# Optimization experiments

Hardware: AMD Instinct MI355X
Metric: run time of the kernel (lower is better)

## Reference

```python
import jax, jax.numpy as jnp
import numpy as np

NUM_NODES = 100000
NUM_EDGES = 1600000
INPUT_DIM = 128
HIDDEN_DIM = 64
OUTPUT_DIM = 2
DROPOUT_P = 0.5


def setup_inputs() -> dict:
    key = jax.random.key(0)
    ks = jax.random.split(key, 6)
    x = jax.random.normal(ks[0], (NUM_NODES, INPUT_DIM), dtype=jnp.float32)
    edge_index = jax.random.randint(ks[1], (2, NUM_EDGES), 0, NUM_NODES, dtype=jnp.int64)
    W_conv = jax.random.normal(ks[2], (INPUT_DIM, HIDDEN_DIM), dtype=jnp.float32) * (1.0 / np.sqrt(INPUT_DIM))
    b_conv = jax.random.normal(ks[3], (HIDDEN_DIM,), dtype=jnp.float32) * 0.02
    W_lin = jax.random.normal(ks[4], (HIDDEN_DIM, OUTPUT_DIM), dtype=jnp.float32) * (1.0 / np.sqrt(HIDDEN_DIM))
    b_lin = jax.random.normal(ks[5], (OUTPUT_DIM,), dtype=jnp.float32) * 0.02
    return {"x": x, "edge_index": edge_index, "W_conv": W_conv, "b_conv": b_conv,
            "W_lin": W_lin, "b_lin": b_lin}


def _gcn_conv(x, edge_index, W, b):
    n = x.shape[0]
    # linear transform first (PyG GCNConv)
    h = x @ W  # [N, hidden]
    # add self-loops
    loop = jnp.arange(n, dtype=edge_index.dtype)
    row = jnp.concatenate([edge_index[0], loop])  # source
    col = jnp.concatenate([edge_index[1], loop])  # target
    # symmetric normalization deg^{-1/2} (degree counted on targets, incl. self-loops)
    deg = jax.ops.segment_sum(jnp.ones_like(col, dtype=h.dtype), col, num_segments=n)
    dinv = jnp.where(deg > 0, jax.lax.rsqrt(deg), 0.0)
    norm = dinv[row] * dinv[col]  # [E+N]
    # gather -> scale -> scatter-add
    msgs = h[row] * norm[:, None]  # [E+N, hidden]
    out = jax.ops.segment_sum(msgs, col, num_segments=n)
    return out + b


def reference(x, edge_index, W_conv, b_conv, W_lin, b_lin):
    h = _gcn_conv(x, edge_index, W_conv, b_conv)
    h = jax.nn.relu(h)
    # dropout p=0.5, training mode, deterministic key for reproducibility
    keep = jax.random.bernoulli(jax.random.key(42), 1.0 - DROPOUT_P, h.shape)
    h = jnp.where(keep, h / (1.0 - DROPOUT_P), 0.0)
    return h @ W_lin + b_lin
```

## Files before the change

### kernel.cpp

```cpp
#include <hip/hip_runtime.h>
#include <hip/hip_bf16.h>

#define N_NODES 100000
#define N_EDGES 1600000
#define IN_DIM 128
#define HID 64
#define NB ((N_NODES + 255) / 256)
#define EPB 4096
#define BUCKET_BLOCKS ((N_EDGES + EPB - 1) / EPB)
#define MAXPB 8192

typedef __attribute__((ext_vector_type(8))) short bf16x8;
typedef __attribute__((ext_vector_type(4))) float f32x4;

__device__ __forceinline__ unsigned rotl32(unsigned x, unsigned r) {
    return (x << r) | (x >> (32u - r));
}

__device__ __forceinline__ void threefry2x32_k42(unsigned x0, unsigned x1,
                                                 unsigned& o0, unsigned& o1) {
    const unsigned ks0 = 0u;
    const unsigned ks1 = 42u;
    const unsigned ks2 = 0u ^ 42u ^ 0x1BD11BDAu;
    x0 += ks0; x1 += ks1;
    x0 += x1; x1 = rotl32(x1, 13); x1 ^= x0;
    x0 += x1; x1 = rotl32(x1, 15); x1 ^= x0;
    x0 += x1; x1 = rotl32(x1, 26); x1 ^= x0;
    x0 += x1; x1 = rotl32(x1, 6);  x1 ^= x0;
    x0 += ks1; x1 += ks2 + 1u;
    x0 += x1; x1 = rotl32(x1, 17); x1 ^= x0;
    x0 += x1; x1 = rotl32(x1, 29); x1 ^= x0;
    x0 += x1; x1 = rotl32(x1, 16); x1 ^= x0;
    x0 += x1; x1 = rotl32(x1, 24); x1 ^= x0;
    x0 += ks2; x1 += ks0 + 2u;
    x0 += x1; x1 = rotl32(x1, 13); x1 ^= x0;
    x0 += x1; x1 = rotl32(x1, 15); x1 ^= x0;
    x0 += x1; x1 = rotl32(x1, 26); x1 ^= x0;
    x0 += x1; x1 = rotl32(x1, 6);  x1 ^= x0;
    x0 += ks0; x1 += ks1 + 3u;
    x0 += x1; x1 = rotl32(x1, 17); x1 ^= x0;
    x0 += x1; x1 = rotl32(x1, 29); x1 ^= x0;
    x0 += x1; x1 = rotl32(x1, 16); x1 ^= x0;
    x0 += x1; x1 = rotl32(x1, 24); x1 ^= x0;
    x0 += ks1; x1 += ks2 + 4u;
    x0 += x1; x1 = rotl32(x1, 13); x1 ^= x0;
    x0 += x1; x1 = rotl32(x1, 15); x1 ^= x0;
    x0 += x1; x1 = rotl32(x1, 26); x1 ^= x0;
    x0 += x1; x1 = rotl32(x1, 6);  x1 ^= x0;
    x0 += ks2; x1 += ks0 + 5u;
    o0 = x0; o1 = x1;
}

__device__ __forceinline__ float bf2f(unsigned short u) {
    return __uint_as_float((unsigned)u << 16);
}
__device__ __forceinline__ float bf2f_lo(unsigned u) {
    return __uint_as_float(u << 16);
}
__device__ __forceinline__ float bf2f_hi(unsigned u) {
    return __uint_as_float(u & 0xffff0000u);
}

__global__ __launch_bounds__(512) void k_bucket(const int* __restrict__ src,
                                                const int* __restrict__ dst,
                                                int* __restrict__ bucketcnt,
                                                unsigned* __restrict__ gbuf) {
    __shared__ int cnt[512];
    __shared__ int off[512];
    __shared__ int cur[NB];
    __shared__ int gbase[NB];
    __shared__ unsigned buf[EPB];
    __shared__ unsigned short bkt[EPB];
    const int t = threadIdx.x;
    const int e0 = blockIdx.x * EPB;
    const int n = min(EPB, N_EDGES - e0);
    cnt[t] = 0;
    __syncthreads();
    unsigned myrec[EPB / 512];
    int myb[EPB / 512];
#pragma unroll
    for (int k = 0; k < EPB / 512; k++) {
        int e = e0 + k * 512 + t;
        if (e < N_EDGES) {
            int r = src[e];
            int c = dst[e];
            int b = c >> 8;
            myrec[k] = ((unsigned)(c & 255) << 17) | (unsigned)r;
            myb[k] = b;
            atomicAdd(&cnt[b], 1);
        } else {
            myb[k] = -1;
        }
    }
    __syncthreads();
    int own = cnt[t];
    for (int o = 1; o < 512; o <<= 1) {
        int v = (t >= o) ? cnt[t - o] : 0;
        __syncthreads();
        cnt[t] += v;
        __syncthreads();
    }
    off[t] = cnt[t] - own;
    if (t < NB) {
        cur[t] = off[t];
        gbase[t] = t * MAXPB + (own ? atomicAdd(&bucketcnt[t], own) : 0);
    }
    __syncthreads();
#pragma unroll
    for (int k = 0; k < EPB / 512; k++) {
        if (myb[k] >= 0) {
            int p = atomicAdd(&cur[myb[k]], 1);
            buf[p] = myrec[k];
            bkt[p] = (unsigned short)myb[k];
        }
    }
    __syncthreads();
    for (int j = t; j < n; j += 512) {
        int b = bkt[j];
        gbuf[gbase[b] + (j - off[b])] = buf[j];
    }
}

__global__ __launch_bounds__(512) void k_scanB(const int* __restrict__ bucketcnt,
                                               int* __restrict__ bucket_base) {
    __shared__ int s[512];
    int t = threadIdx.x;
    int own = (t < NB) ? bucketcnt[t] : 0;
    s[t] = own;
    __syncthreads();
    for (int o = 1; o < 512; o <<= 1) {
        int v = (t >= o) ? s[t - o] : 0;
        __syncthreads();
        s[t] += v;
        __syncthreads();
    }
    if (t < NB) bucket_base[t] = s[t] - own;
    if (t == 511) bucket_base[NB] = s[511];
}

__global__ __launch_bounds__(256) void k_csr2(const unsigned* __restrict__ gbuf,
                                              const int* __restrict__ bucketcnt,
                                              const int* __restrict__ bucket_base,
                                              int* __restrict__ row_start,
                                              float* __restrict__ dinv,
                                              int* __restrict__ srcs) {
    __shared__ unsigned lbuf[MAXPB];
    __shared__ int lcnt[256];
    __shared__ int pre[256];
    __shared__ int cur[256];
    const int b = blockIdx.x, t = threadIdx.x;
    const int n = bucketcnt[b];
    const unsigned* reg = gbuf + (size_t)b * MAXPB;
    lcnt[t] = 0;
    for (int j = t; j < n; j += 256) lbuf[j] = reg[j];
    __syncthreads();
    for (int j = t; j < n; j += 256) atomicAdd(&lcnt[lbuf[j] >> 17], 1);
    __syncthreads();
    int my = lcnt[t];
    pre[t] = my;
    __syncthreads();
    for (int o = 1; o < 256; o <<= 1) {
        int v = (t >= o) ? pre[t - o] : 0;
        __syncthreads();
        pre[t] += v;
        __syncthreads();
    }
    const int gb = bucket_base[b];
    int base = gb + pre[t] - my;
    cur[t] = base;
    const int c = b * 256 + t;
    if (c < N_NODES) {
        row_start[c] = base;
        dinv[c] = rsqrtf((float)(my + 1));
    }
    if (b == NB - 1 && t == 255) row_start[N_NODES] = gb + pre[255];
    __syncthreads();
    for (int j = t; j < n; j += 256) {
        unsigned rec = lbuf[j];
        int pos = atomicAdd(&cur[rec >> 17], 1);
        srcs[pos] = (int)(rec & 0x1FFFF);
    }
}

__global__ __launch_bounds__(256) void k_gemm(const float* __restrict__ x,
                                              const float* __restrict__ W,
                                              const float* __restrict__ dinv,
                                              unsigned short* __restrict__ gm) {
    __shared__ unsigned short WtH[HID][136];
    __shared__ unsigned short WtL[HID][136];
    const int t = threadIdx.x;
    {
        const int n = t & 63;
        const int k0 = (t >> 6) * 32;
        for (int k = k0; k < k0 + 32; k += 2) {
            float w0 = W[(size_t)k * HID + n];
            float w1 = W[(size_t)(k + 1) * HID + n];
            unsigned short h0 = __bfloat16_as_ushort(__float2bfloat16(w0));
            unsigned short h1 = __bfloat16_as_ushort(__float2bfloat16(w1));
            unsigned short l0 = __bfloat16_as_ushort(__float2bfloat16(w0 - bf2f(h0)));
            unsigned short l1 = __bfloat16_as_ushort(__float2bfloat16(w1 - bf2f(h1)));
            *(unsigned*)&WtH[n][k] = (unsigned)h0 | ((unsigned)h1 << 16);
            *(unsigned*)&WtL[n][k] = (unsigned)l0 | ((unsigned)l1 << 16);
        }
    }
    __syncthreads();

    const int wave = t >> 6, lane = t & 63;
    const int row16 = lane & 15;
    const int kgrp = lane >> 4;
    const int browA = blockIdx.x * 64 + wave * 16;

    const int rA = min(browA + row16, N_NODES - 1);
    const float* xr = x + (size_t)rA * IN_DIM + kgrp * 8;
    float xv[32];
#pragma unroll
    for (int ks = 0; ks < 4; ks++) {
        *(f32x4*)&xv[ks * 8]     = *(const f32x4*)(xr + ks * 32);
        *(f32x4*)&xv[ks * 8 + 4] = *(const f32x4*)(xr + ks * 32 + 4);
    }
    bf16x8 ah[4], al[4];
#pragma unroll
    for (int ks = 0; ks < 4; ks++) {
#pragma unroll
        for (int j = 0; j < 8; j++) {
            float v = xv[ks * 8 + j];
            unsigned short h = __bfloat16_as_ushort(__float2bfloat16(v));
            unsigned short l = __bfloat16_as_ushort(__float2bfloat16(v - bf2f(h)));
            ah[ks][j] = (short)h;
            al[ks][j] = (short)l;
        }
    }

    float dv[4];
    int orow[4];
#pragma unroll
    for (int i = 0; i < 4; i++) {
        orow[i] = browA + kgrp * 4 + i;
        dv[i] = dinv[min(orow[i], N_NODES - 1)];
    }

#pragma unroll
    for (int nt = 0; nt < 4; nt++) {
        const int n = nt * 16 + row16;
        bf16x8 bh[4], bl[4];
#pragma unroll
        for (int ks = 0; ks < 4; ks++) {
            bh[ks] = *(const bf16x8*)&WtH[n][ks * 32 + kgrp * 8];
            bl[ks] = *(const bf16x8*)&WtL[n][ks * 32 + kgrp * 8];
        }
        f32x4 acc = {0.f, 0.f, 0.f, 0.f};
#pragma unroll
        for (int ks = 0; ks < 4; ks++)
            acc = __builtin_amdgcn_mfma_f32_16x16x32_bf16(ah[ks], bh[ks], acc, 0, 0, 0);
#pragma unroll
        for (int ks = 0; ks < 4; ks++)
            acc = __builtin_amdgcn_mfma_f32_16x16x32_bf16(al[ks], bh[ks], acc, 0, 0, 0);
#pragma unroll
        for (int ks = 0; ks < 4; ks++)
            acc = __builtin_amdgcn_mfma_f32_16x16x32_bf16(ah[ks], bl[ks], acc, 0, 0, 0);
#pragma unroll
        for (int i = 0; i < 4; i++) {
            if (orow[i] < N_NODES) {
                float g = acc[i] * dv[i];
                gm[(size_t)orow[i] * HID + nt * 16 + row16] =
                    __bfloat16_as_ushort(__float2bfloat16(g));
            }
        }
    }
}

__global__ __launch_bounds__(256, 4) void k_aggr(const unsigned short* __restrict__ gm,
                                                 const int* __restrict__ row_start,
                                                 const int* __restrict__ srcs,
                                                 const float* __restrict__ dinv,
                                                 const float* __restrict__ bconv,
                                                 const float* __restrict__ Wlin,
                                                 const float* __restrict__ blin,
                                                 float* __restrict__ out) {
    const int c  = blockIdx.x * 16 + (threadIdx.x >> 4);
    const int d4 = threadIdx.x & 15;
    const int beg = row_start[c];
    const int end = row_start[c + 1];

    const uint2 s0 = *(const uint2*)(gm + ((size_t)c << 6) + (d4 << 2));
    float a0 = bf2f_lo(s0.x), a1 = bf2f_hi(s0.x);
    float a2 = bf2f_lo(s0.y), a3 = bf2f_hi(s0.y);

#define LOADG(ri) (*(const uint2*)(gm + ((size_t)(ri) << 6) + (d4 << 2)))

    if (beg < end) {
        const int last = end - 1;
        int r[8];
        uint2 wa[8], wb[8];
#pragma unroll
        for (int u = 0; u < 8; u++) r[u] = srcs[min(beg + u, last)];
#pragma unroll
        for (int u = 0; u < 8; u++) wa[u] = LOADG(r[u]);
        bool haveB = (beg + 8 < end);
        if (haveB) {
#pragma unroll
            for (int u = 0; u < 8; u++) r[u] = srcs[min(beg + 8 + u, last)];
#pragma unroll
            for (int u = 0; u < 8; u++) wb[u] = LOADG(r[u]);
        }
        int j = beg;
        while (true) {
#pragma unroll
            for (int u = 0; u < 8; u++) {
                const unsigned m = (j + u < end) ? 0xffffffffu : 0u;
                a0 += bf2f_lo(wa[u].x & m); a1 += bf2f_hi(wa[u].x & m);
                a2 += bf2f_lo(wa[u].y & m); a3 += bf2f_hi(wa[u].y & m);
            }
            j += 8;
            if (!haveB) break;
            const bool haveN = (j + 8 < end);
            if (haveN) {
#pragma unroll
                for (int u = 0; u < 8; u++) r[u] = srcs[min(j + 8 + u, last)];
#pragma unroll
                for (int u = 0; u < 8; u++) wa[u] = LOADG(r[u]);
            }
#pragma unroll
            for (int u = 0; u < 8; u++) {
                const unsigned m = (j + u < end) ? 0xffffffffu : 0u;
                a0 += bf2f_lo(wb[u].x & m); a1 += bf2f_hi(wb[u].x & m);
                a2 += bf2f_lo(wb[u].y & m); a3 += bf2f_hi(wb[u].y & m);
            }
            j += 8;
            if (!haveN) break;
            haveB = (j + 8 < end);
            if (haveB) {
#pragma unroll
                for (int u = 0; u < 8; u++) r[u] = srcs[min(j + 8 + u, last)];
#pragma unroll
                for (int u = 0; u < 8; u++) wb[u] = LOADG(r[u]);
            }
        }
    }
#undef LOADG

    const float dv = dinv[c];
    const float4 bc4 = *(const float4*)(bconv + (d4 << 2));
    float v0 = fmaxf(a0 * dv + bc4.x, 0.f);
    float v1 = fmaxf(a1 * dv + bc4.y, 0.f);
    float v2 = fmaxf(a2 * dv + bc4.z, 0.f);
    float v3 = fmaxf(a3 * dv + bc4.w, 0.f);

    const unsigned ib = (unsigned)(c * HID + (d4 << 2));
    unsigned o0, o1;
    threefry2x32_k42(0u, ib + 0u, o0, o1);
    v0 = ((o0 ^ o1) & 0x80000000u) ? 0.f : v0 * 2.f;
    threefry2x32_k42(0u, ib + 1u, o0, o1);
    v1 = ((o0 ^ o1) & 0x80000000u) ? 0.f : v1 * 2.f;
    threefry2x32_k42(0u, ib + 2u, o0, o1);
    v2 = ((o0 ^ o1) & 0x80000000u) ? 0.f : v2 * 2.f;
    threefry2x32_k42(0u, ib + 3u, o0, o1);
    v3 = ((o0 ^ o1) & 0x80000000u) ? 0.f : v3 * 2.f;

    const float4 wl0 = *(const float4*)(Wlin + (d4 << 3));
    const float4 wl1 = *(const float4*)(Wlin + (d4 << 3) + 4);
    float p0 = v0 * wl0.x + v1 * wl0.z + v2 * wl1.x + v3 * wl1.z;
    float p1 = v0 * wl0.y + v1 * wl0.w + v2 * wl1.y + v3 * wl1.w;

#pragma unroll
    for (int off = 8; off; off >>= 1) {
        p0 += __shfl_xor(p0, off);
        p1 += __shfl_xor(p1, off);
    }
    if (d4 == 0) {
        *(float2*)(out + (size_t)c * 2) = make_float2(p0 + blin[0], p1 + blin[1]);
    }
}

extern "C" void kernel_launch(void* const* d_in, const int* in_sizes, int n_in,
                              void* d_out, int out_size, void* d_ws, size_t ws_size,
                              hipStream_t stream) {
    const float* x  = (const float*)d_in[0];
    const void*  ei = d_in[1];
    const float* Wc = (const float*)d_in[2];
    const float* bc = (const float*)d_in[3];
    const float* Wl = (const float*)d_in[4];
    const float* bl = (const float*)d_in[5];
    for (int i = 0; i < n_in; i++) {
        switch (in_sizes[i]) {
            case N_NODES * IN_DIM:   x  = (const float*)d_in[i]; break;
            case 2 * N_EDGES:
            case 4 * N_EDGES:        ei = d_in[i]; break;
            case IN_DIM * HID:       Wc = (const float*)d_in[i]; break;
            case HID:                bc = (const float*)d_in[i]; break;
            case HID * 2:            Wl = (const float*)d_in[i]; break;
            case 2:                  bl = (const float*)d_in[i]; break;
            default: break;
        }
    }
    float* out = (float*)d_out;

    const int* src = (const int*)ei;
    const int* dst = (const int*)ei + N_EDGES;

    char* ws = (char*)d_ws;
    size_t off = 0;
    unsigned short* gm    = (unsigned short*)(ws + off); off += (size_t)N_NODES * HID * 2;
    float*    dinv        = (float*)(ws + off);    off += (size_t)N_NODES * 4;
    int*      row_start   = (int*)(ws + off);      off += (size_t)(N_NODES + 4) * 4;
    int*      bucketcnt   = (int*)(ws + off);      off += (size_t)(NB + 4) * 4;
    int*      bucket_base = (int*)(ws + off);      off += (size_t)(NB + 4) * 4;
    unsigned* gbuf        = (unsigned*)(ws + off); off += (size_t)NB * MAXPB * 4;
    int*      srcs        = (int*)(ws + off);      off += (size_t)N_EDGES * 4;

    hipMemsetAsync(bucketcnt, 0, (size_t)NB * 4, stream);
    k_bucket<<<BUCKET_BLOCKS, 512, 0, stream>>>(src, dst, bucketcnt, gbuf);
    k_scanB<<<1, 512, 0, stream>>>(bucketcnt, bucket_base);
    k_csr2<<<NB, 256, 0, stream>>>(gbuf, bucketcnt, bucket_base, row_start, dinv, srcs);
    k_gemm<<<(N_NODES + 63) / 64, 256, 0, stream>>>(x, Wc, dinv, gm);
    k_aggr<<<(N_NODES + 15) / 16, 256, 0, stream>>>(gm, row_start, srcs, dinv, bc, Wl, bl, out);
}
```

Measured before the change: 184.2 us.

## Replace block-local bucket sort with global atomic sub-bucket scatter and in-place CSR

```diff
diff --git a/kernel.cpp b/kernel.cpp
--- a/kernel.cpp
+++ b/kernel.cpp
@@ -6,9 +6,9 @@
 #define IN_DIM 128
 #define HID 64
 #define NB ((N_NODES + 255) / 256)
-#define EPB 4096
-#define BUCKET_BLOCKS ((N_EDGES + EPB - 1) / EPB)
-#define MAXPB 8192
+#define NSUB 8
+#define SUBCAP 1024
+#define MAXPB (NSUB * SUBCAP)
 
 typedef __attribute__((ext_vector_type(8))) short bf16x8;
 typedef __attribute__((ext_vector_type(4))) float f32x4;
@@ -61,102 +61,54 @@
     return __uint_as_float(u & 0xffff0000u);
 }
 
-__global__ __launch_bounds__(512) void k_bucket(const int* __restrict__ src,
-                                                const int* __restrict__ dst,
-                                                int* __restrict__ bucketcnt,
-                                                unsigned* __restrict__ gbuf) {
-    __shared__ int cnt[512];
-    __shared__ int off[512];
-    __shared__ int cur[NB];
-    __shared__ int gbase[NB];
-    __shared__ unsigned buf[EPB];
-    __shared__ unsigned short bkt[EPB];
-    const int t = threadIdx.x;
-    const int e0 = blockIdx.x * EPB;
-    const int n = min(EPB, N_EDGES - e0);
-    cnt[t] = 0;
-    __syncthreads();
-    unsigned myrec[EPB / 512];
-    int myb[EPB / 512];
-#pragma unroll
-    for (int k = 0; k < EPB / 512; k++) {
-        int e = e0 + k * 512 + t;
-        if (e < N_EDGES) {
-            int r = src[e];
-            int c = dst[e];
-            int b = c >> 8;
-            myrec[k] = ((unsigned)(c & 255) << 17) | (unsigned)r;
-            myb[k] = b;
-            atomicAdd(&cnt[b], 1);
-        } else {
-            myb[k] = -1;
-        }
-    }
-    __syncthreads();
-    int own = cnt[t];
-    for (int o = 1; o < 512; o <<= 1) {
-        int v = (t >= o) ? cnt[t - o] : 0;
-        __syncthreads();
-        cnt[t] += v;
-        __syncthreads();
-    }
-    off[t] = cnt[t] - own;
-    if (t < NB) {
-        cur[t] = off[t];
-        gbase[t] = t * MAXPB + (own ? atomicAdd(&bucketcnt[t], own) : 0);
-    }
-    __syncthreads();
-#pragma unroll
-    for (int k = 0; k < EPB / 512; k++) {
-        if (myb[k] >= 0) {
-            int p = atomicAdd(&cur[myb[k]], 1);
-            buf[p] = myrec[k];
-            bkt[p] = (unsigned short)myb[k];
-        }
-    }
-    __syncthreads();
-    for (int j = t; j < n; j += 512) {
-        int b = bkt[j];
-        gbuf[gbase[b] + (j - off[b])] = buf[j];
-    }
-}
-
-__global__ __launch_bounds__(512) void k_scanB(const int* __restrict__ bucketcnt,
-                                               int* __restrict__ bucket_base) {
-    __shared__ int s[512];
-    int t = threadIdx.x;
-    int own = (t < NB) ? bucketcnt[t] : 0;
-    s[t] = own;
-    __syncthreads();
-    for (int o = 1; o < 512; o <<= 1) {
-        int v = (t >= o) ? s[t - o] : 0;
-        __syncthreads();
-        s[t] += v;
-        __syncthreads();
-    }
-    if (t < NB) bucket_base[t] = s[t] - own;
-    if (t == 511) bucket_base[NB] = s[511];
-}
-
-__global__ __launch_bounds__(256) void k_csr2(const unsigned* __restrict__ gbuf,
-                                              const int* __restrict__ bucketcnt,
-                                              const int* __restrict__ bucket_base,
-                                              int* __restrict__ row_start,
-                                              float* __restrict__ dinv,
-                                              int* __restrict__ srcs) {
+__global__ __launch_bounds__(256) void k_bucket2(const int* __restrict__ src,
+                                                 const int* __restrict__ dst,
+                                                 int* __restrict__ subcnt,
+                                                 unsigned* __restrict__ gbuf) {
+    const int gid = blockIdx.x * 256 + threadIdx.x;
+    const int e0 = gid * 4;
+    if (e0 >= N_EDGES) return;
+    const int4 s4 = *(const int4*)(src + e0);
+    const int4 d4 = *(const int4*)(dst + e0);
+    const int ss[4] = {s4.x, s4.y, s4.z, s4.w};
+    const int dd[4] = {d4.x, d4.y, d4.z, d4.w};
+#pragma unroll
+    for (int k = 0; k < 4; k++) {
+        const int b = dd[k] >> 8;
+        const int sub = (e0 + k) & (NSUB - 1);
+        const unsigned rec = ((unsigned)(dd[k] & 255) << 17) | (unsigned)ss[k];
+        const int p = atomicAdd(&subcnt[b * NSUB + sub], 1);
+        gbuf[(size_t)b * MAXPB + sub * SUBCAP + p] = rec;
+    }
+}
+
+__global__ __launch_bounds__(256) void k_csr3(unsigned* __restrict__ gbuf,
+                                              const int* __restrict__ subcnt,
+                                              int2* __restrict__ row_se,
+                                              float* __restrict__ dinv) {
     __shared__ unsigned lbuf[MAXPB];
     __shared__ int lcnt[256];
     __shared__ int pre[256];
     __shared__ int cur[256];
+    __shared__ int c8[NSUB + 1];
     const int b = blockIdx.x, t = threadIdx.x;
-    const int n = bucketcnt[b];
-    const unsigned* reg = gbuf + (size_t)b * MAXPB;
+    if (t == 0) {
+        int acc = 0;
+        for (int s = 0; s < NSUB; s++) { c8[s] = acc; acc += subcnt[b * NSUB + s]; }
+        c8[NSUB] = acc;
+    }
     lcnt[t] = 0;
-    for (int j = t; j < n; j += 256) lbuf[j] = reg[j];
+    __syncthreads();
+    for (int s = 0; s < NSUB; s++) {
+        const int n_s = c8[s + 1] - c8[s];
+        const unsigned* seg = gbuf + (size_t)b * MAXPB + s * SUBCAP;
+        for (int j = t; j < n_s; j += 256) lbuf[c8[s] + j] = seg[j];
+    }
+    const int n = c8[NSUB];
     __syncthreads();
     for (int j = t; j < n; j += 256) atomicAdd(&lcnt[lbuf[j] >> 17], 1);
     __syncthreads();
-    int my = lcnt[t];
+    const int my = lcnt[t];
     pre[t] = my;
     __syncthreads();
     for (int o = 1; o < 256; o <<= 1) {
@@ -165,20 +117,18 @@
         pre[t] += v;
         __syncthreads();
     }
-    const int gb = bucket_base[b];
-    int base = gb + pre[t] - my;
+    const int base = b * MAXPB + pre[t] - my;
     cur[t] = base;
     const int c = b * 256 + t;
     if (c < N_NODES) {
-        row_start[c] = base;
+        row_se[c] = make_int2(base, base + my);
         dinv[c] = rsqrtf((float)(my + 1));
     }
-    if (b == NB - 1 && t == 255) row_start[N_NODES] = gb + pre[255];
     __syncthreads();
     for (int j = t; j < n; j += 256) {
-        unsigned rec = lbuf[j];
-        int pos = atomicAdd(&cur[rec >> 17], 1);
-        srcs[pos] = (int)(rec & 0x1FFFF);
+        const unsigned rec = lbuf[j];
+        const int pos = atomicAdd(&cur[rec >> 17], 1);
+        ((int*)gbuf)[pos] = (int)(rec & 0x1FFFF);
     }
 }
 
@@ -270,7 +220,7 @@
 }
 
 __global__ __launch_bounds__(256, 4) void k_aggr(const unsigned short* __restrict__ gm,
-                                                 const int* __restrict__ row_start,
+                                                 const int2* __restrict__ row_se,
                                                  const int* __restrict__ srcs,
                                                  const float* __restrict__ dinv,
                                                  const float* __restrict__ bconv,
@@ -279,8 +229,9 @@
                                                  float* __restrict__ out) {
     const int c  = blockIdx.x * 16 + (threadIdx.x >> 4);
     const int d4 = threadIdx.x & 15;
-    const int beg = row_start[c];
-    const int end = row_start[c + 1];
+    const int2 se = row_se[c];
+    const int beg = se.x;
+    const int end = se.y;
 
     const uint2 s0 = *(const uint2*)(gm + ((size_t)c << 6) + (d4 << 2));
     float a0 = bf2f_lo(s0.x), a1 = bf2f_hi(s0.x);
@@ -400,18 +351,17 @@
 
     char* ws = (char*)d_ws;
     size_t off = 0;
-    unsigned short* gm    = (unsigned short*)(ws + off); off += (size_t)N_NODES * HID * 2;
-    float*    dinv        = (float*)(ws + off);    off += (size_t)N_NODES * 4;
-    int*      row_start   = (int*)(ws + off);      off += (size_t)(N_NODES + 4) * 4;
-    int*      bucketcnt   = (int*)(ws + off);      off += (size_t)(NB + 4) * 4;
-    int*      bucket_base = (int*)(ws + off);      off += (size_t)(NB + 4) * 4;
-    unsigned* gbuf        = (unsigned*)(ws + off); off += (size_t)NB * MAXPB * 4;
-    int*      srcs        = (int*)(ws + off);      off += (size_t)N_EDGES * 4;
-
-    hipMemsetAsync(bucketcnt, 0, (size_t)NB * 4, stream);
-    k_bucket<<<BUCKET_BLOCKS, 512, 0, stream>>>(src, dst, bucketcnt, gbuf);
-    k_scanB<<<1, 512, 0, stream>>>(bucketcnt, bucket_base);
-    k_csr2<<<NB, 256, 0, stream>>>(gbuf, bucketcnt, bucket_base, row_start, dinv, srcs);
+    unsigned short* gm = (unsigned short*)(ws + off); off += (size_t)N_NODES * HID * 2;
+    float* dinv        = (float*)(ws + off);   off += (size_t)N_NODES * 4;
+    int2*  row_se      = (int2*)(ws + off);    off += (size_t)N_NODES * 8;
+    int*   subcnt      = (int*)(ws + off);     off += (size_t)(NB * NSUB + 64) * 4;
+    off = (off + 255) & ~(size_t)255;
+    unsigned* gbuf     = (unsigned*)(ws + off); off += (size_t)NB * MAXPB * 4;
+
+    hipMemsetAsync(subcnt, 0, (size_t)NB * NSUB * 4, stream);
+    k_bucket2<<<(N_EDGES / 4 + 255) / 256, 256, 0, stream>>>(src, dst, subcnt, gbuf);
+    k_csr3<<<NB, 256, 0, stream>>>(gbuf, subcnt, row_se, dinv);
     k_gemm<<<(N_NODES + 63) / 64, 256, 0, stream>>>(x, Wc, dinv, gm);
-    k_aggr<<<(N_NODES + 15) / 16, 256, 0, stream>>>(gm, row_start, srcs, dinv, bc, Wl, bl, out);
-}
+    k_aggr<<<(N_NODES + 15) / 16, 256, 0, stream>>>(gm, row_se, (const int*)gbuf,
+                                                    dinv, bc, Wl, bl, out);
+}
```

New measurement: 310.3 us. 68.5% more time.

## Drop bucket scan kernel, build sparse CSR in place with start/end pairs

Applied to the files above, without the earlier changes.

```diff
diff --git a/kernel.cpp b/kernel.cpp
--- a/kernel.cpp
+++ b/kernel.cpp
@@ -121,29 +121,10 @@
     }
 }
 
-__global__ __launch_bounds__(512) void k_scanB(const int* __restrict__ bucketcnt,
-                                               int* __restrict__ bucket_base) {
-    __shared__ int s[512];
-    int t = threadIdx.x;
-    int own = (t < NB) ? bucketcnt[t] : 0;
-    s[t] = own;
-    __syncthreads();
-    for (int o = 1; o < 512; o <<= 1) {
-        int v = (t >= o) ? s[t - o] : 0;
-        __syncthreads();
-        s[t] += v;
-        __syncthreads();
-    }
-    if (t < NB) bucket_base[t] = s[t] - own;
-    if (t == 511) bucket_base[NB] = s[511];
-}
-
-__global__ __launch_bounds__(256) void k_csr2(const unsigned* __restrict__ gbuf,
+__global__ __launch_bounds__(256) void k_csr3(unsigned* __restrict__ gbuf,
                                               const int* __restrict__ bucketcnt,
-                                              const int* __restrict__ bucket_base,
-                                              int* __restrict__ row_start,
-                                              float* __restrict__ dinv,
-                                              int* __restrict__ srcs) {
+                                              int2* __restrict__ row_se,
+                                              float* __restrict__ dinv) {
     __shared__ unsigned lbuf[MAXPB];
     __shared__ int lcnt[256];
     __shared__ int pre[256];
@@ -156,7 +137,7 @@
     __syncthreads();
     for (int j = t; j < n; j += 256) atomicAdd(&lcnt[lbuf[j] >> 17], 1);
     __syncthreads();
-    int my = lcnt[t];
+    const int my = lcnt[t];
     pre[t] = my;
     __syncthreads();
     for (int o = 1; o < 256; o <<= 1) {
@@ -165,20 +146,18 @@
         pre[t] += v;
         __syncthreads();
     }
-    const int gb = bucket_base[b];
-    int base = gb + pre[t] - my;
+    const int base = b * MAXPB + pre[t] - my;
     cur[t] = base;
     const int c = b * 256 + t;
     if (c < N_NODES) {
-        row_start[c] = base;
+        row_se[c] = make_int2(base, base + my);
         dinv[c] = rsqrtf((float)(my + 1));
     }
-    if (b == NB - 1 && t == 255) row_start[N_NODES] = gb + pre[255];
     __syncthreads();
     for (int j = t; j < n; j += 256) {
-        unsigned rec = lbuf[j];
-        int pos = atomicAdd(&cur[rec >> 17], 1);
-        srcs[pos] = (int)(rec & 0x1FFFF);
+        const unsigned rec = lbuf[j];
+        const int pos = atomicAdd(&cur[rec >> 17], 1);
+        ((int*)gbuf)[pos] = (int)(rec & 0x1FFFF);
     }
 }
 
@@ -270,7 +249,7 @@
 }
 
 __global__ __launch_bounds__(256, 4) void k_aggr(const unsigned short* __restrict__ gm,
-                                                 const int* __restrict__ row_start,
+                                                 const int2* __restrict__ row_se,
                                                  const int* __restrict__ srcs,
                                                  const float* __restrict__ dinv,
                                                  const float* __restrict__ bconv,
@@ -279,8 +258,9 @@
                                                  float* __restrict__ out) {
     const int c  = blockIdx.x * 16 + (threadIdx.x >> 4);
     const int d4 = threadIdx.x & 15;
-    const int beg = row_start[c];
-    const int end = row_start[c + 1];
+    const int2 se = row_se[c];
+    const int beg = se.x;
+    const int end = se.y;
 
     const uint2 s0 = *(const uint2*)(gm + ((size_t)c << 6) + (d4 << 2));
     float a0 = bf2f_lo(s0.x), a1 = bf2f_hi(s0.x);
@@ -400,18 +380,17 @@
 
     char* ws = (char*)d_ws;
     size_t off = 0;
-    unsigned short* gm    = (unsigned short*)(ws + off); off += (size_t)N_NODES * HID * 2;
-    float*    dinv        = (float*)(ws + off);    off += (size_t)N_NODES * 4;
-    int*      row_start   = (int*)(ws + off);      off += (size_t)(N_NODES + 4) * 4;
-    int*      bucketcnt   = (int*)(ws + off);      off += (size_t)(NB + 4) * 4;
-    int*      bucket_base = (int*)(ws + off);      off += (size_t)(NB + 4) * 4;
-    unsigned* gbuf        = (unsigned*)(ws + off); off += (size_t)NB * MAXPB * 4;
-    int*      srcs        = (int*)(ws + off);      off += (size_t)N_EDGES * 4;
+    unsigned short* gm = (unsigned short*)(ws + off); off += (size_t)N_NODES * HID * 2;
+    float* dinv        = (float*)(ws + off);   off += (size_t)N_NODES * 4;
+    int2*  row_se      = (int2*)(ws + off);    off += (size_t)N_NODES * 8;
+    int*   bucketcnt   = (int*)(ws + off);     off += (size_t)(NB + 64) * 4;
+    off = (off + 255) & ~(size_t)255;
+    unsigned* gbuf     = (unsigned*)(ws + off); off += (size_t)NB * MAXPB * 4;
 
     hipMemsetAsync(bucketcnt, 0, (size_t)NB * 4, stream);
     k_bucket<<<BUCKET_BLOCKS, 512, 0, stream>>>(src, dst, bucketcnt, gbuf);
-    k_scanB<<<1, 512, 0, stream>>>(bucketcnt, bucket_base);
-    k_csr2<<<NB, 256, 0, stream>>>(gbuf, bucketcnt, bucket_base, row_start, dinv, srcs);
+    k_csr3<<<NB, 256, 0, stream>>>(gbuf, bucketcnt, row_se, dinv);
     k_gemm<<<(N_NODES + 63) / 64, 256, 0, stream>>>(x, Wc, dinv, gm);
-    k_aggr<<<(N_NODES + 15) / 16, 256, 0, stream>>>(gm, row_start, srcs, dinv, bc, Wl, bl, out);
-}
+    k_aggr<<<(N_NODES + 15) / 16, 256, 0, stream>>>(gm, row_se, (const int*)gbuf,
+                                                    dinv, bc, Wl, bl, out);
+}
```

Result: faster. 174.5 us (-5.3%).
